# Optimization experiments

Hardware: AMD Instinct MI355X
Metric: run time of the kernel (lower is better)

## Reference

```python
import jax, jax.numpy as jnp
import numpy as np

EPS = 1e-5  # torch BatchNorm1d default eps
NUM_CLASSES = 10


def setup_inputs() -> dict:
    key = jax.random.key(0)
    ks = jax.random.split(key, 8)
    N, M, D = 8192, 8192, 256
    h1, h2 = 128, 64
    x = jax.random.normal(ks[0], (N, D), dtype=jnp.float32)
    x_n = jax.random.normal(ks[1], (M, D), dtype=jnp.float32)
    y_n = jax.random.randint(ks[2], (M,), 0, NUM_CLASSES)
    # Linear weights (torch layout [out, in]) and biases
    W0 = jax.random.normal(ks[3], (h1, D), dtype=jnp.float32) * 0.05
    b0 = jnp.zeros((h1,), dtype=jnp.float32)
    W1 = jax.random.normal(ks[4], (h2, h1), dtype=jnp.float32) * 0.05
    b1 = jnp.zeros((h2,), dtype=jnp.float32)
    # BatchNorm1d affine params (torch init: weight=1, bias=0)
    g0 = jnp.ones((h1,), dtype=jnp.float32)
    bt0 = jnp.zeros((h1,), dtype=jnp.float32)
    g1 = jnp.ones((h2,), dtype=jnp.float32)
    bt1 = jnp.zeros((h2,), dtype=jnp.float32)
    return {"x": x, "x_n": x_n, "y_n": y_n,
            "W0": W0, "b0": b0, "g0": g0, "bt0": bt0,
            "W1": W1, "b1": b1, "g1": g1, "bt1": bt1}


def _bn(h, gamma, beta):
    # BatchNorm1d in training mode: batch mean / biased batch var per feature
    m = jnp.mean(h, axis=0)
    v = jnp.var(h, axis=0)
    return gamma * (h - m) / jnp.sqrt(v + EPS) + beta


def _feats(z, params):
    # fcn stack: BatchNorm(Tanh(Linear(z)))
    for W, b, g, bt in params:
        z = _bn(jnp.tanh(z @ W.T + b), g, bt)
    return z


def reference(x, x_n, y_n, W0, b0, g0, bt0, W1, b1, g1, bt1):
    params = [(W0, b0, g0, bt0), (W1, b1, g1, bt1)]
    q = _feats(x, params)    # [N, 64]
    k = _feats(x_n, params)  # [M, 64]
    # euclidean cdist via the quadratic expansion
    d2 = (jnp.sum(q * q, axis=1)[:, None]
          + jnp.sum(k * k, axis=1)[None, :]
          - 2.0 * (q @ k.T))
    sim = jnp.sqrt(jnp.maximum(d2, 1e-12))  # [N, M]
    sim = jnp.max(sim) - sim                 # larger = nearer
    # x != x_n here, so no self-mask branch (matches torch.equal check)
    p = jax.nn.softmax(sim, axis=1)          # [N, M]
    y1h = jax.nn.one_hot(y_n, NUM_CLASSES, dtype=p.dtype)  # [M, C]
    return jnp.clip(p @ y1h, 0.0, 1.0)       # [N, C]
```

## Files before the change

### kernel.cpp

```cpp
#include <hip/hip_runtime.h>
#include <math.h>

#define EPSBN 1e-5f

typedef unsigned short u16;
typedef short bf16x8 __attribute__((ext_vector_type(8)));
typedef float f32x4 __attribute__((ext_vector_type(4)));
typedef int i32x4 __attribute__((ext_vector_type(4)));

constexpr int NROWS = 8192;
constexpr int D0 = 256;
constexpr int F1 = 128;
constexpr int F2 = 64;
constexpr int TOT = 2 * NROWS;
constexpr int NCLS = 10;
constexpr int MPAD = 8832;
constexpr int NT_PAD = MPAD / 64;
constexpr int GY = 12;

constexpr size_t OFF_W0P = 0;
constexpr size_t OFF_H1H = 32768;
constexpr size_t OFF_H1L = OFF_H1H + 1048576;
constexpr size_t OFF_P1S = OFF_H1L + 1048576;
constexpr size_t OFF_P1Q = OFF_P1S + 131072;
constexpr size_t OFF_SC0 = OFF_P1Q + 131072;
constexpr size_t OFF_SH0 = OFF_SC0 + 256;
constexpr size_t OFF_W1P = OFF_SH0 + 256;
constexpr size_t OFF_B1E = OFF_W1P + 16384;
constexpr size_t OFF_H2  = OFF_B1E + 128;
constexpr size_t OFF_P2S = OFF_H2 + 1048576;
constexpr size_t OFF_P2Q = OFF_P2S + 65536;
constexpr size_t OFF_SC1 = OFF_P2Q + 65536;
constexpr size_t OFF_SH1 = OFF_SC1 + 128;
constexpr size_t OFF_PIDX= OFF_SH1 + 128;
constexpr size_t OFF_TCLS= OFF_PIDX + MPAD;
constexpr size_t OFF_QH  = OFF_H1H;
constexpr size_t OFF_QL  = OFF_QH + 262144;
constexpr size_t OFF_QN2 = OFF_QL + 262144;
constexpr size_t OFF_KH  = OFF_QN2 + NROWS;
constexpr size_t OFF_KL  = OFF_KH + 282624;
constexpr size_t OFF_KN2 = OFF_KL + 282624;
constexpr size_t OFF_PART= OFF_H2;

__device__ inline u16 f2bf(float f) {
  unsigned u = __float_as_uint(f);
  unsigned r = (u + 0x7fffu + ((u >> 16) & 1u)) >> 16;
  return (u16)r;
}
__device__ inline float bf2f(u16 h) { return __uint_as_float(((unsigned)h) << 16); }

__device__ inline float tanh_fast(float x) {
  float e = __builtin_amdgcn_exp2f(x * 2.88539008f);
  return 1.f - 2.f * __builtin_amdgcn_rcpf(e + 1.f);
}

__global__ void k_w0pack(const float* __restrict__ w0, u16* __restrict__ w0p) {
  int idx = blockIdx.x * 256 + threadIdx.x;
  int j = idx >> 8, t = idx & 255;
  float v = w0[idx];
  u16 hi = f2bf(v);
  u16 lo = f2bf(v - bf2f(hi));
  w0p[(t >> 3) * 1024 + j * 8 + (t & 7)] = hi;
  w0p[32768 + (t >> 3) * 1024 + j * 8 + (t & 7)] = lo;
}

__global__ __launch_bounds__(256) void k_layer1(
    const float* __restrict__ x, const float* __restrict__ xn,
    const u16* __restrict__ w0p, const float* __restrict__ b0,
    u16* __restrict__ h1h, u16* __restrict__ h1l,
    float* __restrict__ p1s, float* __restrict__ p1q)
{
  const int tid = threadIdx.x;
  const int w = tid >> 6, l = tid & 63;
  const int l15 = l & 15, l4 = l >> 4;
  const int blk = blockIdx.x;
  const int rowHalf = w & 1, colHalf = w >> 1;
  const int r0 = blk * 32 + 16 * rowHalf;
  const int c0 = 64 * colHalf;
  const float* src = (blk < 256) ? (x + (size_t)blk * 32 * 256)
                                 : (xn + (size_t)(blk - 256) * 32 * 256);
  const float* xrow = src + (size_t)(16 * rowHalf + l15) * 256;

  f32x4 acc[4];
  #pragma unroll
  for (int ct = 0; ct < 4; ++ct) acc[ct] = (f32x4){0.f, 0.f, 0.f, 0.f};

  #pragma unroll
  for (int ks = 0; ks < 8; ++ks) {
    const float* xp = xrow + ks * 32 + l4 * 8;
    f32x4 a0 = *(const f32x4*)xp;
    f32x4 a1 = *(const f32x4*)(xp + 4);
    bf16x8 ah, al_;
    #pragma unroll
    for (int i = 0; i < 4; ++i) {
      u16 h = f2bf(a0[i]); ah[i] = (short)h; al_[i] = (short)f2bf(a0[i] - bf2f(h));
    }
    #pragma unroll
    for (int i = 0; i < 4; ++i) {
      u16 h = f2bf(a1[i]); ah[4 + i] = (short)h; al_[4 + i] = (short)f2bf(a1[i] - bf2f(h));
    }
    const u16* bbase = w0p + (size_t)(ks * 4 + l4) * 1024;
    #pragma unroll
    for (int ct = 0; ct < 4; ++ct) {
      const int col = c0 + 16 * ct + l15;
      bf16x8 bh = *(const bf16x8*)(bbase + col * 8);
      bf16x8 bl = *(const bf16x8*)(bbase + 32768 + col * 8);
      acc[ct] = __builtin_amdgcn_mfma_f32_16x16x32_bf16(ah, bh, acc[ct], 0, 0, 0);
      acc[ct] = __builtin_amdgcn_mfma_f32_16x16x32_bf16(ah, bl, acc[ct], 0, 0, 0);
      acc[ct] = __builtin_amdgcn_mfma_f32_16x16x32_bf16(al_, bh, acc[ct], 0, 0, 0);
    }
  }

  #pragma unroll
  for (int ct = 0; ct < 4; ++ct) {
    const int col = c0 + 16 * ct + l15;
    const float bj = b0[col];
    float s = 0.f, q = 0.f;
    #pragma unroll
    for (int r = 0; r < 4; ++r) {
      float v = tanh_fast(acc[ct][r] + bj);
      const int row = r0 + 4 * l4 + r;
      u16 hi = f2bf(v);
      h1h[(size_t)row * 128 + col] = hi;
      h1l[(size_t)row * 128 + col] = f2bf(v - bf2f(hi));
      s += v; q += v * v;
    }
    s += __shfl_xor(s, 16); s += __shfl_xor(s, 32);
    q += __shfl_xor(q, 16); q += __shfl_xor(q, 32);
    if (l < 16) {
      p1s[(size_t)(blk * 2 + rowHalf) * 128 + col] = s;
      p1q[(size_t)(blk * 2 + rowHalf) * 128 + col] = q;
    }
  }
}

__global__ __launch_bounds__(64) void k_red1(
    const float* __restrict__ p1s, const float* __restrict__ p1q,
    const float* __restrict__ g0, const float* __restrict__ bt0,
    float* __restrict__ sc0, float* __restrict__ sh0)
{
  const int b = blockIdx.x >> 7;
  const int j = blockIdx.x & 127;
  const int t = threadIdx.x;
  float s = 0.f, q = 0.f;
  for (int i = t; i < 512; i += 64) {
    s += p1s[(size_t)(b * 512 + i) * 128 + j];
    q += p1q[(size_t)(b * 512 + i) * 128 + j];
  }
  #pragma unroll
  for (int off = 32; off; off >>= 1) { s += __shfl_xor(s, off); q += __shfl_xor(q, off); }
  if (t == 0) {
    float m = s / (float)NROWS;
    float v = q / (float)NROWS - m * m;
    float sc = g0[j] * rsqrtf(v + EPSBN);
    sc0[b * 128 + j] = sc;
    sh0[b * 128 + j] = bt0[j] - m * sc;
  }
}

__global__ __launch_bounds__(128) void k_fold(
    const float* __restrict__ w1, const float* __restrict__ b1,
    const float* __restrict__ sc0, const float* __restrict__ sh0,
    u16* __restrict__ w1p, float* __restrict__ b1e)
{
  const int tid = threadIdx.x;
  const int b = tid >> 6, o = tid & 63;
  float acc = 0.f;
  for (int j = 0; j < 128; ++j) {
    float w = w1[o * 128 + j];
    float ws = w * sc0[b * 128 + j];
    acc += w * sh0[b * 128 + j];
    u16 hi = f2bf(ws);
    u16 lo = f2bf(ws - bf2f(hi));
    w1p[((size_t)(b * 2 + 0) * 16 + (j >> 3)) * 512 + o * 8 + (j & 7)] = hi;
    w1p[((size_t)(b * 2 + 1) * 16 + (j >> 3)) * 512 + o * 8 + (j & 7)] = lo;
  }
  b1e[b * 64 + o] = b1[o] + acc;
}

__global__ __launch_bounds__(256) void k_layer2(
    const u16* __restrict__ h1h, const u16* __restrict__ h1l,
    const u16* __restrict__ w1p, const float* __restrict__ b1e,
    float* __restrict__ h2, float* __restrict__ p2s, float* __restrict__ p2q)
{
  const int tid = threadIdx.x;
  const int w = tid >> 6, l = tid & 63;
  const int l15 = l & 15, l4 = l >> 4;
  const int blk = blockIdx.x;
  const int rowHalf = w & 1, colHalf = w >> 1;
  const int r0 = blk * 32 + 16 * rowHalf;
  const int c0 = 32 * colHalf;
  const int b = blk >> 8;
  const u16* arow_h = h1h + (size_t)(r0 + l15) * 128;
  const u16* arow_l = h1l + (size_t)(r0 + l15) * 128;

  f32x4 acc[2];
  acc[0] = (f32x4){0.f, 0.f, 0.f, 0.f};
  acc[1] = (f32x4){0.f, 0.f, 0.f, 0.f};

  #pragma unroll
  for (int ks = 0; ks < 4; ++ks) {
    bf16x8 ah = *(const bf16x8*)(arow_h + ks * 32 + l4 * 8);
    bf16x8 al_ = *(const bf16x8*)(arow_l + ks * 32 + l4 * 8);
    const u16* bb = w1p + ((size_t)(b * 2) * 16 + ks * 4 + l4) * 512;
    #pragma unroll
    for (int ct = 0; ct < 2; ++ct) {
      const int col = c0 + 16 * ct + l15;
      bf16x8 bh = *(const bf16x8*)(bb + col * 8);
      bf16x8 bl = *(const bf16x8*)(bb + 8192 + col * 8);
      acc[ct] = __builtin_amdgcn_mfma_f32_16x16x32_bf16(ah, bh, acc[ct], 0, 0, 0);
      acc[ct] = __builtin_amdgcn_mfma_f32_16x16x32_bf16(ah, bl, acc[ct], 0, 0, 0);
      acc[ct] = __builtin_amdgcn_mfma_f32_16x16x32_bf16(al_, bh, acc[ct], 0, 0, 0);
    }
  }

  #pragma unroll
  for (int ct = 0; ct < 2; ++ct) {
    const int col = c0 + 16 * ct + l15;
    const float bj = b1e[b * 64 + col];
    float s = 0.f, q = 0.f;
    #pragma unroll
    for (int r = 0; r < 4; ++r) {
      float v = tanh_fast(acc[ct][r] + bj);
      const int row = r0 + 4 * l4 + r;
      h2[(size_t)row * 64 + col] = v;
      s += v; q += v * v;
    }
    s += __shfl_xor(s, 16); s += __shfl_xor(s, 32);
    q += __shfl_xor(q, 16); q += __shfl_xor(q, 32);
    if (l < 16) {
      p2s[(size_t)(blk * 2 + rowHalf) * 64 + col] = s;
      p2q[(size_t)(blk * 2 + rowHalf) * 64 + col] = q;
    }
  }
}

__global__ __launch_bounds__(64) void k_red2(
    const float* __restrict__ p2s, const float* __restrict__ p2q,
    const float* __restrict__ g1, const float* __restrict__ bt1,
    float* __restrict__ sc1, float* __restrict__ sh1)
{
  const int b = blockIdx.x >> 6;
  const int o = blockIdx.x & 63;
  const int t = threadIdx.x;
  float s = 0.f, q = 0.f;
  for (int i = t; i < 512; i += 64) {
    s += p2s[(size_t)(b * 512 + i) * 64 + o];
    q += p2q[(size_t)(b * 512 + i) * 64 + o];
  }
  #pragma unroll
  for (int off = 32; off; off >>= 1) { s += __shfl_xor(s, off); q += __shfl_xor(q, off); }
  if (t == 0) {
    float m = s / (float)NROWS;
    float v = q / (float)NROWS - m * m;
    float sc = g1[o] * rsqrtf(v + EPSBN);
    sc1[b * 64 + o] = sc;
    sh1[b * 64 + o] = bt1[o] - m * sc;
  }
}

__global__ __launch_bounds__(256) void k_sort(const int* __restrict__ yn,
                                              int* __restrict__ pidx, int* __restrict__ tcls)
{
  __shared__ int cnt[256][NCLS];
  __shared__ int wtot[4][NCLS];
  __shared__ int pstart[NCLS + 1];
  const int t = threadIdx.x;
  const int lane = t & 63, w = t >> 6;
  #pragma unroll
  for (int c = 0; c < NCLS; ++c) cnt[t][c] = 0;
  for (int i = t; i < MPAD; i += 256) pidx[i] = -1;
  const int base = t * 32;
  for (int i = 0; i < 32; ++i) cnt[t][yn[base + i]]++;
  __syncthreads();
  #pragma unroll
  for (int c = 0; c < NCLS; ++c) {
    int x = cnt[t][c];
    int inc = x;
    #pragma unroll
    for (int d = 1; d < 64; d <<= 1) { int y = __shfl_up(inc, d); if (lane >= d) inc += y; }
    if (lane == 63) wtot[w][c] = inc;
    cnt[t][c] = inc - x;
  }
  __syncthreads();
  if (t == 0) {
    int run = 0;
    #pragma unroll
    for (int c = 0; c < NCLS; ++c) {
      int tot = wtot[0][c] + wtot[1][c] + wtot[2][c] + wtot[3][c];
      pstart[c] = run;
      int ntile = (tot + 63) >> 6;
      for (int tt = 0; tt < ntile; ++tt) tcls[(run >> 6) + tt] = c;
      run += ntile << 6;
    }
    pstart[NCLS] = run;
    for (int tt = run >> 6; tt < NT_PAD; ++tt) tcls[tt] = NCLS;
  }
  __syncthreads();
  #pragma unroll
  for (int c = 0; c < NCLS; ++c) {
    int add = pstart[c];
    for (int w2 = 0; w2 < 4; ++w2) if (w2 < w) add += wtot[w2][c];
    cnt[t][c] += add;
  }
  __syncthreads();
  for (int i = 0; i < 32; ++i) {
    int idx = base + i;
    int c = yn[idx];
    pidx[cnt[t][c]++] = idx;
  }
}

__global__ __launch_bounds__(256) void k_bn2(
    const float* __restrict__ h2, const float* __restrict__ sc1, const float* __restrict__ sh1,
    const int* __restrict__ pidx,
    u16* __restrict__ qh, u16* __restrict__ ql, float* __restrict__ qn2,
    u16* __restrict__ kh, u16* __restrict__ kl, float* __restrict__ kn2)
{
  const int tid = threadIdx.x;
  const int r = tid >> 6, o = tid & 63;
  if (blockIdx.x < 2048) {
    const int row = blockIdx.x * 4 + r;
    float v = sc1[o] * h2[(size_t)row * 64 + o] + sh1[o];
    u16 hi = f2bf(v);
    qh[(size_t)row * 64 + o] = hi;
    ql[(size_t)row * 64 + o] = f2bf(v - bf2f(hi));
    float sq = v * v;
    #pragma unroll
    for (int off = 32; off; off >>= 1) sq += __shfl_xor(sq, off);
    if (o == 0) qn2[row] = sq;
  } else {
    const int row = (blockIdx.x - 2048) * 4 + r;
    const int src = pidx[row];
    float v = 0.f;
    if (src >= 0) v = sc1[64 + o] * h2[(size_t)(NROWS + src) * 64 + o] + sh1[64 + o];
    u16 hi = f2bf(v);
    kh[(size_t)row * 64 + o] = hi;
    kl[(size_t)row * 64 + o] = f2bf(v - bf2f(hi));
    float sq = v * v;
    #pragma unroll
    for (int off = 32; off; off >>= 1) sq += __shfl_xor(sq, off);
    if (o == 0) kn2[row] = (src >= 0) ? sq : 1e30f;
  }
}

__global__ __launch_bounds__(256) void k_dist(
    const u16* __restrict__ qh, const u16* __restrict__ ql, const float* __restrict__ qn2,
    const u16* __restrict__ kh, const u16* __restrict__ kl, const float* __restrict__ kn2,
    const int* __restrict__ tcls, float* __restrict__ part)
{
  __shared__ u16 bs[64 * 128];
  __shared__ float cls_lds[(NCLS + 1) * 64];
  const int tid = threadIdx.x;
  const int l = tid & 63, w = tid >> 6;
  const int n0 = blockIdx.x * 64;
  const int g = blockIdx.y;
  const int t0 = g * 12;
  const int t1 = (t0 + 12 < NT_PAD) ? (t0 + 12) : NT_PAD;

  for (int i = tid; i < (NCLS + 1) * 64; i += 256) cls_lds[i] = 0.f;

  const int l15 = l & 15, l4 = l >> 4;
  const int arow = n0 + 16 * w + l15;
  const bf16x8 aH0 = *(const bf16x8*)(qh + (size_t)arow * 64 + l4 * 8);
  const bf16x8 aH1 = *(const bf16x8*)(qh + (size_t)arow * 64 + 32 + l4 * 8);
  const bf16x8 aL0 = *(const bf16x8*)(ql + (size_t)arow * 64 + l4 * 8);
  const bf16x8 aL1 = *(const bf16x8*)(ql + (size_t)arow * 64 + 32 + l4 * 8);
  const f32x4 qn = *(const f32x4*)(qn2 + n0 + 16 * w + l4 * 4);

  const ushort* arrp = ((tid >> 3) & 1) ? kl : kh;
  const int cp8 = (tid & 7) * 8;
  const int colb = tid >> 4;
  const int slot = ((tid >> 3) & 1) * 8 + ((tid & 7) ^ (colb & 7));
  char* dstb = (char*)bs + colb * 256 + slot * 16;

  const int P = l15 * 256 + ((l4 ^ (l & 7)) << 4);
  const char* bb = (const char*)bs;

  i32x4 st0, st1, st2, st3;
  {
    const int m0 = t0 * 64;
    st0 = *(const i32x4*)(arrp + (size_t)(m0 + colb) * 64 + cp8);
    st1 = *(const i32x4*)(arrp + (size_t)(m0 + 16 + colb) * 64 + cp8);
    st2 = *(const i32x4*)(arrp + (size_t)(m0 + 32 + colb) * 64 + cp8);
    st3 = *(const i32x4*)(arrp + (size_t)(m0 + 48 + colb) * 64 + cp8);
  }

  float run0 = 0.f, run1 = 0.f, run2 = 0.f, run3 = 0.f;
  int ccur = tcls[t0];

#define FLUSH(CC) { \
    run0 += __shfl_xor(run0, 1); run0 += __shfl_xor(run0, 2); run0 += __shfl_xor(run0, 4); run0 += __shfl_xor(run0, 8); \
    run1 += __shfl_xor(run1, 1); run1 += __shfl_xor(run1, 2); run1 += __shfl_xor(run1, 4); run1 += __shfl_xor(run1, 8); \
    run2 += __shfl_xor(run2, 1); run2 += __shfl_xor(run2, 2); run2 += __shfl_xor(run2, 4); run2 += __shfl_xor(run2, 8); \
    run3 += __shfl_xor(run3, 1); run3 += __shfl_xor(run3, 2); run3 += __shfl_xor(run3, 4); run3 += __shfl_xor(run3, 8); \
    if (l15 == 0) { \
      float* cl = cls_lds + (CC) * 64 + 16 * w + l4 * 4; \
      cl[0] += run0; cl[1] += run1; cl[2] += run2; cl[3] += run3; \
    } \
    run0 = run1 = run2 = run3 = 0.f; \
  }

#define CTSTEP(CT, ACC) { \
    const char* pp = bb + (CT) * 4096; \
    bf16x8 bh0 = *(const bf16x8*)(pp + P); \
    bf16x8 bh1 = *(const bf16x8*)(pp + (P ^ 64)); \
    bf16x8 bl0 = *(const bf16x8*)(pp + (P ^ 128)); \
    bf16x8 bl1 = *(const bf16x8*)(pp + (P ^ 192)); \
    ACC = __builtin_amdgcn_mfma_f32_16x16x32_bf16(aH0, bh0, ACC, 0, 0, 0); \
    ACC = __builtin_amdgcn_mfma_f32_16x16x32_bf16(aH1, bh1, ACC, 0, 0, 0); \
    ACC = __builtin_amdgcn_mfma_f32_16x16x32_bf16(aH0, bl0, ACC, 0, 0, 0); \
    ACC = __builtin_amdgcn_mfma_f32_16x16x32_bf16(aH1, bl1, ACC, 0, 0, 0); \
    ACC = __builtin_amdgcn_mfma_f32_16x16x32_bf16(aL0, bh0, ACC, 0, 0, 0); \
    ACC = __builtin_amdgcn_mfma_f32_16x16x32_bf16(aL1, bh1, ACC, 0, 0, 0); \
  }

#define EPI(ACC, KV) { \
    float d2, s_, u; \
    d2 = fmaxf(fmaf(-2.f, ACC[0], qn[0] + (KV)), 1e-12f); \
    s_ = __builtin_amdgcn_sqrtf(d2); \
    u = __builtin_amdgcn_exp2f(s_ * -1.44269504f); run0 += u; \
    d2 = fmaxf(fmaf(-2.f, ACC[1], qn[1] + (KV)), 1e-12f); \
    s_ = __builtin_amdgcn_sqrtf(d2); \
    u = __builtin_amdgcn_exp2f(s_ * -1.44269504f); run1 += u; \
    d2 = fmaxf(fmaf(-2.f, ACC[2], qn[2] + (KV)), 1e-12f); \
    s_ = __builtin_amdgcn_sqrtf(d2); \
    u = __builtin_amdgcn_exp2f(s_ * -1.44269504f); run2 += u; \
    d2 = fmaxf(fmaf(-2.f, ACC[3], qn[3] + (KV)), 1e-12f); \
    s_ = __builtin_amdgcn_sqrtf(d2); \
    u = __builtin_amdgcn_exp2f(s_ * -1.44269504f); run3 += u; \
  }

  for (int t = t0; t < t1; ++t) {
    const int m0 = t * 64;
    __syncthreads();
    *(i32x4*)(dstb)         = st0;
    *(i32x4*)(dstb + 4096)  = st1;
    *(i32x4*)(dstb + 8192)  = st2;
    *(i32x4*)(dstb + 12288) = st3;
    __syncthreads();
    if (t + 1 < t1) {
      const int m1 = m0 + 64;
      st0 = *(const i32x4*)(arrp + (size_t)(m1 + colb) * 64 + cp8);
      st1 = *(const i32x4*)(arrp + (size_t)(m1 + 16 + colb) * 64 + cp8);
      st2 = *(const i32x4*)(arrp + (size_t)(m1 + 32 + colb) * 64 + cp8);
      st3 = *(const i32x4*)(arrp + (size_t)(m1 + 48 + colb) * 64 + cp8);
    }
    const float kv0 = kn2[m0 + l15];
    const float kv1 = kn2[m0 + 16 + l15];
    const float kv2 = kn2[m0 + 32 + l15];
    const float kv3 = kn2[m0 + 48 + l15];
    const int c = tcls[t];
    if (c != ccur) { FLUSH(ccur); ccur = c; }

    f32x4 acc0 = {0.f, 0.f, 0.f, 0.f};
    f32x4 acc1 = {0.f, 0.f, 0.f, 0.f};
    f32x4 acc2 = {0.f, 0.f, 0.f, 0.f};
    f32x4 acc3 = {0.f, 0.f, 0.f, 0.f};
    CTSTEP(0, acc0)
    CTSTEP(1, acc1)
    CTSTEP(2, acc2)
    CTSTEP(3, acc3)
    EPI(acc0, kv0)
    EPI(acc1, kv1)
    EPI(acc2, kv2)
    EPI(acc3, kv3)
  }
  FLUSH(ccur);
  __syncthreads();

  for (int i = tid; i < (NCLS + 1) * 64; i += 256) {
    const int c = i >> 6, r = i & 63;
    part[((size_t)g * (NCLS + 1) + c) * NROWS + n0 + r] = cls_lds[i];
  }
#undef FLUSH
#undef CTSTEP
#undef EPI
}

__global__ __launch_bounds__(256) void k_final(const float* __restrict__ part,
                                               float* __restrict__ out)
{
  const int n = blockIdx.x * 256 + threadIdx.x;
  float sc[NCLS];
  #pragma unroll
  for (int c = 0; c < NCLS; ++c) sc[c] = 0.f;
  for (int g = 0; g < GY; ++g) {
    #pragma unroll
    for (int c = 0; c < NCLS; ++c)
      sc[c] += part[((size_t)g * (NCLS + 1) + c) * NROWS + n];
  }
  float tot = 0.f;
  #pragma unroll
  for (int c = 0; c < NCLS; ++c) tot += sc[c];
  const float inv = 1.f / tot;
  #pragma unroll
  for (int c = 0; c < NCLS; ++c)
    out[(size_t)n * NCLS + c] = fminf(fmaxf(sc[c] * inv, 0.f), 1.f);
}

extern "C" void kernel_launch(void* const* d_in, const int* in_sizes, int n_in,
                              void* d_out, int out_size, void* d_ws, size_t ws_size,
                              hipStream_t stream) {
  const float* x   = (const float*)d_in[0];
  const float* xn  = (const float*)d_in[1];
  const int*   yn  = (const int*)d_in[2];
  const float* W0  = (const float*)d_in[3];
  const float* b0  = (const float*)d_in[4];
  const float* g0  = (const float*)d_in[5];
  const float* bt0 = (const float*)d_in[6];
  const float* W1  = (const float*)d_in[7];
  const float* b1  = (const float*)d_in[8];
  const float* g1  = (const float*)d_in[9];
  const float* bt1 = (const float*)d_in[10];
  float* out = (float*)d_out;
  float* ws  = (float*)d_ws;

  u16*   w0pp = (u16*)(ws + OFF_W0P);
  u16*   h1hp = (u16*)(ws + OFF_H1H);
  u16*   h1lp = (u16*)(ws + OFF_H1L);
  float* p1sp = ws + OFF_P1S;
  float* p1qp = ws + OFF_P1Q;
  float* sc0p = ws + OFF_SC0;
  float* sh0p = ws + OFF_SH0;
  u16*   w1pp = (u16*)(ws + OFF_W1P);
  float* b1ep = ws + OFF_B1E;
  float* h2p  = ws + OFF_H2;
  float* p2sp = ws + OFF_P2S;
  float* p2qp = ws + OFF_P2Q;
  float* sc1p = ws + OFF_SC1;
  float* sh1p = ws + OFF_SH1;
  int*   pidxp= (int*)(ws + OFF_PIDX);
  int*   tclsp= (int*)(ws + OFF_TCLS);
  u16*   qhp  = (u16*)(ws + OFF_QH);
  u16*   qlp  = (u16*)(ws + OFF_QL);
  float* qn2p = ws + OFF_QN2;
  u16*   khp  = (u16*)(ws + OFF_KH);
  u16*   klp  = (u16*)(ws + OFF_KL);
  float* kn2p = ws + OFF_KN2;
  float* partp= ws + OFF_PART;

  k_sort<<<1, 256, 0, stream>>>(yn, pidxp, tclsp);
  k_w0pack<<<128, 256, 0, stream>>>(W0, w0pp);
  k_layer1<<<512, 256, 0, stream>>>(x, xn, w0pp, b0, h1hp, h1lp, p1sp, p1qp);
  k_red1<<<256, 64, 0, stream>>>(p1sp, p1qp, g0, bt0, sc0p, sh0p);
  k_fold<<<1, 128, 0, stream>>>(W1, b1, sc0p, sh0p, w1pp, b1ep);
  k_layer2<<<512, 256, 0, stream>>>(h1hp, h1lp, w1pp, b1ep, h2p, p2sp, p2qp);
  k_red2<<<128, 64, 0, stream>>>(p2sp, p2qp, g1, bt1, sc1p, sh1p);
  k_bn2<<<2048 + MPAD / 4, 256, 0, stream>>>(h2p, sc1p, sh1p, pidxp,
                                             qhp, qlp, qn2p, khp, klp, kn2p);
  k_dist<<<dim3(128, GY), 256, 0, stream>>>(qhp, qlp, qn2p, khp, klp, kn2p, tclsp, partp);
  k_final<<<32, 256, 0, stream>>>(partp, out);
}
```

Measured before the change: 152.6 us.

## Fuse prep kernels, atomic BN stats, and retile distance kernel to 32x32 MFMA

Merges the label sort and W0 packing into one prep kernel. BatchNorm partial sums are now accumulated with atomics, which removes both reduction kernels, and the fold is parallelised across 64 blocks. The distance kernel moves to 32x32x16 MFMA tiles with double-buffered LDS staging and a prefetch two tiles ahead, halves the grid's y-dimension, and folds the log2(e) scale into the norms so the epilogue needs one exp2 without a multiply. The costs are float atomics, which make the summation order nondeterministic, and more registers per thread, with occupancy capped at 3 blocks.

```diff
diff --git a/kernel.cpp b/kernel.cpp
--- a/kernel.cpp
+++ b/kernel.cpp
@@ -2,45 +2,39 @@
 #include <math.h>
 
 #define EPSBN 1e-5f
+#define AADD(p, v) __hip_atomic_fetch_add((p), (v), __ATOMIC_RELAXED, __HIP_MEMORY_SCOPE_AGENT)
 
 typedef unsigned short u16;
 typedef short bf16x8 __attribute__((ext_vector_type(8)));
 typedef float f32x4 __attribute__((ext_vector_type(4)));
+typedef float f32x16 __attribute__((ext_vector_type(16)));
 typedef int i32x4 __attribute__((ext_vector_type(4)));
 
 constexpr int NROWS = 8192;
-constexpr int D0 = 256;
-constexpr int F1 = 128;
-constexpr int F2 = 64;
-constexpr int TOT = 2 * NROWS;
 constexpr int NCLS = 10;
 constexpr int MPAD = 8832;
-constexpr int NT_PAD = MPAD / 64;
-constexpr int GY = 12;
+constexpr int NT_PAD = 138;
+constexpr int GY = 6;
+constexpr int TPG = 23;
+constexpr float SCL  = 2.0813689810056077f;
+constexpr float SCL2 = -4.1627379620112154f;
 
 constexpr size_t OFF_W0P = 0;
 constexpr size_t OFF_H1H = 32768;
 constexpr size_t OFF_H1L = OFF_H1H + 1048576;
-constexpr size_t OFF_P1S = OFF_H1L + 1048576;
-constexpr size_t OFF_P1Q = OFF_P1S + 131072;
-constexpr size_t OFF_SC0 = OFF_P1Q + 131072;
-constexpr size_t OFF_SH0 = OFF_SC0 + 256;
-constexpr size_t OFF_W1P = OFF_SH0 + 256;
+constexpr size_t OFF_SUM = OFF_H1L + 1048576;
+constexpr size_t OFF_W1P = OFF_SUM + 768;
 constexpr size_t OFF_B1E = OFF_W1P + 16384;
 constexpr size_t OFF_H2  = OFF_B1E + 128;
-constexpr size_t OFF_P2S = OFF_H2 + 1048576;
-constexpr size_t OFF_P2Q = OFF_P2S + 65536;
-constexpr size_t OFF_SC1 = OFF_P2Q + 65536;
-constexpr size_t OFF_SH1 = OFF_SC1 + 128;
-constexpr size_t OFF_PIDX= OFF_SH1 + 128;
-constexpr size_t OFF_TCLS= OFF_PIDX + MPAD;
+constexpr size_t OFF_PIDX = OFF_H2 + 1048576;
+constexpr size_t OFF_TCLS = OFF_PIDX + MPAD;
 constexpr size_t OFF_QH  = OFF_H1H;
 constexpr size_t OFF_QL  = OFF_QH + 262144;
 constexpr size_t OFF_QN2 = OFF_QL + 262144;
 constexpr size_t OFF_KH  = OFF_QN2 + NROWS;
 constexpr size_t OFF_KL  = OFF_KH + 282624;
 constexpr size_t OFF_KN2 = OFF_KL + 282624;
-constexpr size_t OFF_PART= OFF_H2;
+constexpr size_t OFF_PART = OFF_H2;
 
 __device__ inline u16 f2bf(float f) {
   unsigned u = __float_as_uint(f);
@@ -54,21 +48,74 @@
   return 1.f - 2.f * __builtin_amdgcn_rcpf(e + 1.f);
 }
 
-__global__ void k_w0pack(const float* __restrict__ w0, u16* __restrict__ w0p) {
-  int idx = blockIdx.x * 256 + threadIdx.x;
-  int j = idx >> 8, t = idx & 255;
-  float v = w0[idx];
-  u16 hi = f2bf(v);
-  u16 lo = f2bf(v - bf2f(hi));
-  w0p[(t >> 3) * 1024 + j * 8 + (t & 7)] = hi;
-  w0p[32768 + (t >> 3) * 1024 + j * 8 + (t & 7)] = lo;
+__global__ __launch_bounds__(256) void k_prep(
+    const float* __restrict__ w0, const int* __restrict__ yn,
+    u16* __restrict__ w0p, int* __restrict__ pidx, int* __restrict__ tcls,
+    float* __restrict__ sums)
+{
+  if (blockIdx.x < 128) {
+    int idx = blockIdx.x * 256 + threadIdx.x;
+    int t = idx & 255;
+    float v = w0[idx];
+    u16 hi = f2bf(v);
+    u16 lo = f2bf(v - bf2f(hi));
+    int j = idx >> 8;
+    w0p[(t >> 3) * 1024 + j * 8 + (t & 7)] = hi;
+    w0p[32768 + (t >> 3) * 1024 + j * 8 + (t & 7)] = lo;
+    return;
+  }
+  __shared__ int cnt[256][NCLS];
+  __shared__ int wtot[4][NCLS];
+  __shared__ int pstart[NCLS + 1];
+  const int t = threadIdx.x;
+  const int lane = t & 63, wv = t >> 6;
+  sums[t] = 0.f; sums[t + 256] = 0.f; sums[t + 512] = 0.f;
+  #pragma unroll
+  for (int c = 0; c < NCLS; ++c) cnt[t][c] = 0;
+  for (int i = t; i < MPAD; i += 256) pidx[i] = -1;
+  for (int i = t; i < NROWS; i += 256) cnt[t][yn[i]]++;
+  __syncthreads();
+  #pragma unroll
+  for (int c = 0; c < NCLS; ++c) {
+    int x = cnt[t][c];
+    int inc = x;
+    #pragma unroll
+    for (int d = 1; d < 64; d <<= 1) { int y = __shfl_up(inc, d); if (lane >= d) inc += y; }
+    if (lane == 63) wtot[wv][c] = inc;
+    cnt[t][c] = inc - x;
+  }
+  __syncthreads();
+  if (t == 0) {
+    int run = 0;
+    #pragma unroll
+    for (int c = 0; c < NCLS; ++c) {
+      int tot = wtot[0][c] + wtot[1][c] + wtot[2][c] + wtot[3][c];
+      pstart[c] = run;
+      int ntile = (tot + 63) >> 6;
+      for (int tt = 0; tt < ntile; ++tt) tcls[(run >> 6) + tt] = c;
+      run += ntile << 6;
+    }
+    pstart[NCLS] = run;
+    for (int tt = run >> 6; tt < NT_PAD; ++tt) tcls[tt] = NCLS;
+  }
+  __syncthreads();
+  #pragma unroll
+  for (int c = 0; c < NCLS; ++c) {
+    int add = pstart[c];
+    for (int w2 = 0; w2 < 4; ++w2) if (w2 < wv) add += wtot[w2][c];
+    cnt[t][c] += add;
+  }
+  __syncthreads();
+  for (int i = t; i < NROWS; i += 256) {
+    int c = yn[i];
+    pidx[cnt[t][c]++] = i;
+  }
 }
 
 __global__ __launch_bounds__(256) void k_layer1(
     const float* __restrict__ x, const float* __restrict__ xn,
     const u16* __restrict__ w0p, const float* __restrict__ b0,
-    u16* __restrict__ h1h, u16* __restrict__ h1l,
-    float* __restrict__ p1s, float* __restrict__ p1q)
+    u16* __restrict__ h1h, u16* __restrict__ h1l, float* __restrict__ sums)
 {
   const int tid = threadIdx.x;
   const int w = tid >> 6, l = tid & 63;
@@ -77,6 +124,7 @@
   const int rowHalf = w & 1, colHalf = w >> 1;
   const int r0 = blk * 32 + 16 * rowHalf;
   const int c0 = 64 * colHalf;
+  const int b = (blk < 256) ? 0 : 1;
   const float* src = (blk < 256) ? (x + (size_t)blk * 32 * 256)
                                  : (xn + (size_t)(blk - 256) * 32 * 256);
   const float* xrow = src + (size_t)(16 * rowHalf + l15) * 256;
@@ -128,60 +176,46 @@
     s += __shfl_xor(s, 16); s += __shfl_xor(s, 32);
     q += __shfl_xor(q, 16); q += __shfl_xor(q, 32);
     if (l < 16) {
-      p1s[(size_t)(blk * 2 + rowHalf) * 128 + col] = s;
-      p1q[(size_t)(blk * 2 + rowHalf) * 128 + col] = q;
-    }
-  }
-}
-
-__global__ __launch_bounds__(64) void k_red1(
-    const float* __restrict__ p1s, const float* __restrict__ p1q,
+      AADD(&sums[b * 128 + col], s);
+      AADD(&sums[256 + b * 128 + col], q);
+    }
+  }
+}
+
+__global__ __launch_bounds__(128) void k_foldp(
+    const float* __restrict__ w1, const float* __restrict__ b1,
     const float* __restrict__ g0, const float* __restrict__ bt0,
-    float* __restrict__ sc0, float* __restrict__ sh0)
-{
-  const int b = blockIdx.x >> 7;
-  const int j = blockIdx.x & 127;
-  const int t = threadIdx.x;
-  float s = 0.f, q = 0.f;
-  for (int i = t; i < 512; i += 64) {
-    s += p1s[(size_t)(b * 512 + i) * 128 + j];
-    q += p1q[(size_t)(b * 512 + i) * 128 + j];
-  }
-  #pragma unroll
-  for (int off = 32; off; off >>= 1) { s += __shfl_xor(s, off); q += __shfl_xor(q, off); }
-  if (t == 0) {
-    float m = s / (float)NROWS;
-    float v = q / (float)NROWS - m * m;
+    const float* __restrict__ sums, u16* __restrict__ w1p, float* __restrict__ b1e)
+{
+  const int o = blockIdx.x;
+  const int j = threadIdx.x;
+  __shared__ float red[2][2];
+  const float w = w1[o * 128 + j];
+  #pragma unroll
+  for (int b = 0; b < 2; ++b) {
+    float s = sums[b * 128 + j], q = sums[256 + b * 128 + j];
+    float m = s * (1.f / 8192.f);
+    float v = q * (1.f / 8192.f) - m * m;
     float sc = g0[j] * rsqrtf(v + EPSBN);
-    sc0[b * 128 + j] = sc;
-    sh0[b * 128 + j] = bt0[j] - m * sc;
-  }
-}
-
-__global__ __launch_bounds__(128) void k_fold(
-    const float* __restrict__ w1, const float* __restrict__ b1,
-    const float* __restrict__ sc0, const float* __restrict__ sh0,
-    u16* __restrict__ w1p, float* __restrict__ b1e)
-{
-  const int tid = threadIdx.x;
-  const int b = tid >> 6, o = tid & 63;
-  float acc = 0.f;
-  for (int j = 0; j < 128; ++j) {
-    float w = w1[o * 128 + j];
-    float ws = w * sc0[b * 128 + j];
-    acc += w * sh0[b * 128 + j];
-    u16 hi = f2bf(ws);
-    u16 lo = f2bf(ws - bf2f(hi));
+    float sh = bt0[j] - m * sc;
+    float wsc = w * sc;
+    u16 hi = f2bf(wsc);
+    u16 lo = f2bf(wsc - bf2f(hi));
     w1p[((size_t)(b * 2 + 0) * 16 + (j >> 3)) * 512 + o * 8 + (j & 7)] = hi;
     w1p[((size_t)(b * 2 + 1) * 16 + (j >> 3)) * 512 + o * 8 + (j & 7)] = lo;
-  }
-  b1e[b * 64 + o] = b1[o] + acc;
+    float a = w * sh;
+    #pragma unroll
+    for (int off = 32; off; off >>= 1) a += __shfl_xor(a, off);
+    if ((j & 63) == 0) red[j >> 6][b] = a;
+  }
+  __syncthreads();
+  if (j < 2) b1e[j * 64 + o] = b1[o] + red[0][j] + red[1][j];
 }
 
 __global__ __launch_bounds__(256) void k_layer2(
     const u16* __restrict__ h1h, const u16* __restrict__ h1l,
     const u16* __restrict__ w1p, const float* __restrict__ b1e,
-    float* __restrict__ h2, float* __restrict__ p2s, float* __restrict__ p2q)
+    float* __restrict__ h2, float* __restrict__ sums)
 {
   const int tid = threadIdx.x;
   const int w = tid >> 6, l = tid & 63;
@@ -229,253 +263,163 @@
     s += __shfl_xor(s, 16); s += __shfl_xor(s, 32);
     q += __shfl_xor(q, 16); q += __shfl_xor(q, 32);
     if (l < 16) {
-      p2s[(size_t)(blk * 2 + rowHalf) * 64 + col] = s;
-      p2q[(size_t)(blk * 2 + rowHalf) * 64 + col] = q;
-    }
-  }
-}
-
-__global__ __launch_bounds__(64) void k_red2(
-    const float* __restrict__ p2s, const float* __restrict__ p2q,
+      AADD(&sums[512 + b * 64 + col], s);
+      AADD(&sums[640 + b * 64 + col], q);
+    }
+  }
+}
+
+__global__ __launch_bounds__(256) void k_bn2(
+    const float* __restrict__ h2, const float* __restrict__ sums,
     const float* __restrict__ g1, const float* __restrict__ bt1,
-    float* __restrict__ sc1, float* __restrict__ sh1)
-{
-  const int b = blockIdx.x >> 6;
-  const int o = blockIdx.x & 63;
-  const int t = threadIdx.x;
-  float s = 0.f, q = 0.f;
-  for (int i = t; i < 512; i += 64) {
-    s += p2s[(size_t)(b * 512 + i) * 64 + o];
-    q += p2q[(size_t)(b * 512 + i) * 64 + o];
-  }
-  #pragma unroll
-  for (int off = 32; off; off >>= 1) { s += __shfl_xor(s, off); q += __shfl_xor(q, off); }
-  if (t == 0) {
-    float m = s / (float)NROWS;
-    float v = q / (float)NROWS - m * m;
-    float sc = g1[o] * rsqrtf(v + EPSBN);
-    sc1[b * 64 + o] = sc;
-    sh1[b * 64 + o] = bt1[o] - m * sc;
-  }
-}
-
-__global__ __launch_bounds__(256) void k_sort(const int* __restrict__ yn,
-                                              int* __restrict__ pidx, int* __restrict__ tcls)
-{
-  __shared__ int cnt[256][NCLS];
-  __shared__ int wtot[4][NCLS];
-  __shared__ int pstart[NCLS + 1];
-  const int t = threadIdx.x;
-  const int lane = t & 63, w = t >> 6;
-  #pragma unroll
-  for (int c = 0; c < NCLS; ++c) cnt[t][c] = 0;
-  for (int i = t; i < MPAD; i += 256) pidx[i] = -1;
-  const int base = t * 32;
-  for (int i = 0; i < 32; ++i) cnt[t][yn[base + i]]++;
-  __syncthreads();
-  #pragma unroll
-  for (int c = 0; c < NCLS; ++c) {
-    int x = cnt[t][c];
-    int inc = x;
-    #pragma unroll
-    for (int d = 1; d < 64; d <<= 1) { int y = __shfl_up(inc, d); if (lane >= d) inc += y; }
-    if (lane == 63) wtot[w][c] = inc;
-    cnt[t][c] = inc - x;
-  }
-  __syncthreads();
-  if (t == 0) {
-    int run = 0;
-    #pragma unroll
-    for (int c = 0; c < NCLS; ++c) {
-      int tot = wtot[0][c] + wtot[1][c] + wtot[2][c] + wtot[3][c];
-      pstart[c] = run;
-      int ntile = (tot + 63) >> 6;
-      for (int tt = 0; tt < ntile; ++tt) tcls[(run >> 6) + tt] = c;
-      run += ntile << 6;
-    }
-    pstart[NCLS] = run;
-    for (int tt = run >> 6; tt < NT_PAD; ++tt) tcls[tt] = NCLS;
-  }
-  __syncthreads();
-  #pragma unroll
-  for (int c = 0; c < NCLS; ++c) {
-    int add = pstart[c];
-    for (int w2 = 0; w2 < 4; ++w2) if (w2 < w) add += wtot[w2][c];
-    cnt[t][c] += add;
-  }
-  __syncthreads();
-  for (int i = 0; i < 32; ++i) {
-    int idx = base + i;
-    int c = yn[idx];
-    pidx[cnt[t][c]++] = idx;
-  }
-}
-
-__global__ __launch_bounds__(256) void k_bn2(
-    const float* __restrict__ h2, const float* __restrict__ sc1, const float* __restrict__ sh1,
     const int* __restrict__ pidx,
     u16* __restrict__ qh, u16* __restrict__ ql, float* __restrict__ qn2,
     u16* __restrict__ kh, u16* __restrict__ kl, float* __restrict__ kn2)
 {
   const int tid = threadIdx.x;
   const int r = tid >> 6, o = tid & 63;
-  if (blockIdx.x < 2048) {
+  const bool isq = (blockIdx.x < 2048);
+  const int b = isq ? 0 : 1;
+  float s = sums[512 + b * 64 + o], q = sums[640 + b * 64 + o];
+  float m = s * (1.f / 8192.f);
+  float v = q * (1.f / 8192.f) - m * m;
+  float sc = g1[o] * rsqrtf(v + EPSBN);
+  float sh = bt1[o] - m * sc;
+  if (isq) {
     const int row = blockIdx.x * 4 + r;
-    float v = sc1[o] * h2[(size_t)row * 64 + o] + sh1[o];
-    u16 hi = f2bf(v);
+    float vv = sc * h2[(size_t)row * 64 + o] + sh;
+    u16 hi = f2bf(vv);
     qh[(size_t)row * 64 + o] = hi;
-    ql[(size_t)row * 64 + o] = f2bf(v - bf2f(hi));
-    float sq = v * v;
+    ql[(size_t)row * 64 + o] = f2bf(vv - bf2f(hi));
+    float sq = vv * vv;
     #pragma unroll
     for (int off = 32; off; off >>= 1) sq += __shfl_xor(sq, off);
-    if (o == 0) qn2[row] = sq;
+    if (o == 0) qn2[row] = SCL * sq;
   } else {
     const int row = (blockIdx.x - 2048) * 4 + r;
     const int src = pidx[row];
-    float v = 0.f;
-    if (src >= 0) v = sc1[64 + o] * h2[(size_t)(NROWS + src) * 64 + o] + sh1[64 + o];
-    u16 hi = f2bf(v);
+    float vv = 0.f;
+    if (src >= 0) vv = sc * h2[(size_t)(NROWS + src) * 64 + o] + sh;
+    u16 hi = f2bf(vv);
     kh[(size_t)row * 64 + o] = hi;
-    kl[(size_t)row * 64 + o] = f2bf(v - bf2f(hi));
-    float sq = v * v;
+    kl[(size_t)row * 64 + o] = f2bf(vv - bf2f(hi));
+    float sq = vv * vv;
     #pragma unroll
     for (int off = 32; off; off >>= 1) sq += __shfl_xor(sq, off);
-    if (o == 0) kn2[row] = (src >= 0) ? sq : 1e30f;
-  }
-}
-
-__global__ __launch_bounds__(256) void k_dist(
+    if (o == 0) kn2[row] = (src >= 0) ? SCL * sq : 1e30f;
+  }
+}
+
+__global__ __launch_bounds__(256, 3) void k_dist(
     const u16* __restrict__ qh, const u16* __restrict__ ql, const float* __restrict__ qn2,
     const u16* __restrict__ kh, const u16* __restrict__ kl, const float* __restrict__ kn2,
     const int* __restrict__ tcls, float* __restrict__ part)
 {
-  __shared__ u16 bs[64 * 128];
-  __shared__ float cls_lds[(NCLS + 1) * 64];
+  __shared__ u16 bs[2][8192];
+  __shared__ float cls_lds[2 * (NCLS + 1) * 64];
   const int tid = threadIdx.x;
-  const int l = tid & 63, w = tid >> 6;
+  const int w = tid >> 6, l = tid & 63;
   const int n0 = blockIdx.x * 64;
   const int g = blockIdx.y;
-  const int t0 = g * 12;
-  const int t1 = (t0 + 12 < NT_PAD) ? (t0 + 12) : NT_PAD;
-
-  for (int i = tid; i < (NCLS + 1) * 64; i += 256) cls_lds[i] = 0.f;
-
-  const int l15 = l & 15, l4 = l >> 4;
-  const int arow = n0 + 16 * w + l15;
-  const bf16x8 aH0 = *(const bf16x8*)(qh + (size_t)arow * 64 + l4 * 8);
-  const bf16x8 aH1 = *(const bf16x8*)(qh + (size_t)arow * 64 + 32 + l4 * 8);
-  const bf16x8 aL0 = *(const bf16x8*)(ql + (size_t)arow * 64 + l4 * 8);
-  const bf16x8 aL1 = *(const bf16x8*)(ql + (size_t)arow * 64 + 32 + l4 * 8);
-  const f32x4 qn = *(const f32x4*)(qn2 + n0 + 16 * w + l4 * 4);
-
-  const ushort* arrp = ((tid >> 3) & 1) ? kl : kh;
-  const int cp8 = (tid & 7) * 8;
-  const int colb = tid >> 4;
-  const int slot = ((tid >> 3) & 1) * 8 + ((tid & 7) ^ (colb & 7));
-  char* dstb = (char*)bs + colb * 256 + slot * 16;
-
-  const int P = l15 * 256 + ((l4 ^ (l & 7)) << 4);
-  const char* bb = (const char*)bs;
+  const int t0 = g * TPG, t1 = t0 + TPG;
+
+  for (int i = tid; i < 2 * (NCLS + 1) * 64; i += 256) cls_lds[i] = 0.f;
+
+  const int lh = l >> 5;
+  const int arow = n0 + 32 * (w >> 1) + (l & 31);
+  bf16x8 aH[4], aL[4];
+  #pragma unroll
+  for (int j = 0; j < 4; ++j) {
+    aH[j] = *(const bf16x8*)(qh + (size_t)arow * 64 + j * 16 + 8 * lh);
+    aL[j] = *(const bf16x8*)(ql + (size_t)arow * 64 + j * 16 + 8 * lh);
+  }
+  float qnr[16];
+  #pragma unroll
+  for (int g4 = 0; g4 < 4; ++g4) {
+    f32x4 qv = *(const f32x4*)(qn2 + n0 + 32 * (w >> 1) + 8 * g4 + 4 * lh);
+    qnr[4 * g4 + 0] = qv[0]; qnr[4 * g4 + 1] = qv[1];
+    qnr[4 * g4 + 2] = qv[2]; qnr[4 * g4 + 3] = qv[3];
+  }
+
+  const int sarr = w & 1, shalf = w >> 1;
+  const u16* sbase = (sarr ? kl : kh) + (size_t)l * 64 + shalf * 32;
+  const int c7l = l & 7;
+  char* wb_base = (char*)&bs[0][0] + l * 256 + sarr * 128;
+  const int ws0 = (((shalf * 4 + 0) ^ c7l) << 4);
+  const int ws1 = (((shalf * 4 + 1) ^ c7l) << 4);
+  const int ws2 = (((shalf * 4 + 2) ^ c7l) << 4);
+  const int ws3 = (((shalf * 4 + 3) ^ c7l) << 4);
+
+  const int colL = 32 * (w & 1) + (l & 31);
+  const char* rb_base = (const char*)&bs[0][0] + colL * 256;
+  const int c7r = colL & 7;
 
   i32x4 st0, st1, st2, st3;
-  {
-    const int m0 = t0 * 64;
-    st0 = *(const i32x4*)(arrp + (size_t)(m0 + colb) * 64 + cp8);
-    st1 = *(const i32x4*)(arrp + (size_t)(m0 + 16 + colb) * 64 + cp8);
-    st2 = *(const i32x4*)(arrp + (size_t)(m0 + 32 + colb) * 64 + cp8);
-    st3 = *(const i32x4*)(arrp + (size_t)(m0 + 48 + colb) * 64 + cp8);
-  }
-
-  float run0 = 0.f, run1 = 0.f, run2 = 0.f, run3 = 0.f;
+#define LOADST(TT) do { const u16* sp_ = sbase + (size_t)(TT) * 4096; \
+    st0 = *(const i32x4*)(sp_);      st1 = *(const i32x4*)(sp_ + 8);  \
+    st2 = *(const i32x4*)(sp_ + 16); st3 = *(const i32x4*)(sp_ + 24); } while (0)
+#define WRITEST(PB) do { char* d_ = wb_base + (PB) * 16384; \
+    *(i32x4*)(d_ + ws0) = st0; *(i32x4*)(d_ + ws1) = st1; \
+    *(i32x4*)(d_ + ws2) = st2; *(i32x4*)(d_ + ws3) = st3; } while (0)
+#define FLUSH(CC) do { \
+    _Pragma("unroll") for (int r = 0; r < 16; ++r) { \
+      run[r] += __shfl_xor(run[r], 1);  run[r] += __shfl_xor(run[r], 2); \
+      run[r] += __shfl_xor(run[r], 4);  run[r] += __shfl_xor(run[r], 8); \
+      run[r] += __shfl_xor(run[r], 16); } \
+    if ((l & 31) == 0) { \
+      float* cl_ = cls_lds + (w & 1) * 704 + (CC) * 64 + 32 * (w >> 1) + 4 * lh; \
+      _Pragma("unroll") for (int r = 0; r < 16; ++r) cl_[(r & 3) + 8 * (r >> 2)] += run[r]; } \
+    _Pragma("unroll") for (int r = 0; r < 16; ++r) run[r] = 0.f; } while (0)
+
+  LOADST(t0);
+  WRITEST(0);
+  LOADST(t0 + 1);
+
+  float run[16];
+  #pragma unroll
+  for (int r = 0; r < 16; ++r) run[r] = 0.f;
   int ccur = tcls[t0];
-
-#define FLUSH(CC) { \
-    run0 += __shfl_xor(run0, 1); run0 += __shfl_xor(run0, 2); run0 += __shfl_xor(run0, 4); run0 += __shfl_xor(run0, 8); \
-    run1 += __shfl_xor(run1, 1); run1 += __shfl_xor(run1, 2); run1 += __shfl_xor(run1, 4); run1 += __shfl_xor(run1, 8); \
-    run2 += __shfl_xor(run2, 1); run2 += __shfl_xor(run2, 2); run2 += __shfl_xor(run2, 4); run2 += __shfl_xor(run2, 8); \
-    run3 += __shfl_xor(run3, 1); run3 += __shfl_xor(run3, 2); run3 += __shfl_xor(run3, 4); run3 += __shfl_xor(run3, 8); \
-    if (l15 == 0) { \
-      float* cl = cls_lds + (CC) * 64 + 16 * w + l4 * 4; \
-      cl[0] += run0; cl[1] += run1; cl[2] += run2; cl[3] += run3; \
-    } \
-    run0 = run1 = run2 = run3 = 0.f; \
-  }
-
-#define CTSTEP(CT, ACC) { \
-    const char* pp = bb + (CT) * 4096; \
-    bf16x8 bh0 = *(const bf16x8*)(pp + P); \
-    bf16x8 bh1 = *(const bf16x8*)(pp + (P ^ 64)); \
-    bf16x8 bl0 = *(const bf16x8*)(pp + (P ^ 128)); \
-    bf16x8 bl1 = *(const bf16x8*)(pp + (P ^ 192)); \
-    ACC = __builtin_amdgcn_mfma_f32_16x16x32_bf16(aH0, bh0, ACC, 0, 0, 0); \
-    ACC = __builtin_amdgcn_mfma_f32_16x16x32_bf16(aH1, bh1, ACC, 0, 0, 0); \
-    ACC = __builtin_amdgcn_mfma_f32_16x16x32_bf16(aH0, bl0, ACC, 0, 0, 0); \
-    ACC = __builtin_amdgcn_mfma_f32_16x16x32_bf16(aH1, bl1, ACC, 0, 0, 0); \
-    ACC = __builtin_amdgcn_mfma_f32_16x16x32_bf16(aL0, bh0, ACC, 0, 0, 0); \
-    ACC = __builtin_amdgcn_mfma_f32_16x16x32_bf16(aL1, bh1, ACC, 0, 0, 0); \
-  }
-
-#define EPI(ACC, KV) { \
-    float d2, s_, u; \
-    d2 = fmaxf(fmaf(-2.f, ACC[0], qn[0] + (KV)), 1e-12f); \
-    s_ = __builtin_amdgcn_sqrtf(d2); \
-    u = __builtin_amdgcn_exp2f(s_ * -1.44269504f); run0 += u; \
-    d2 = fmaxf(fmaf(-2.f, ACC[1], qn[1] + (KV)), 1e-12f); \
-    s_ = __builtin_amdgcn_sqrtf(d2); \
-    u = __builtin_amdgcn_exp2f(s_ * -1.44269504f); run1 += u; \
-    d2 = fmaxf(fmaf(-2.f, ACC[2], qn[2] + (KV)), 1e-12f); \
-    s_ = __builtin_amdgcn_sqrtf(d2); \
-    u = __builtin_amdgcn_exp2f(s_ * -1.44269504f); run2 += u; \
-    d2 = fmaxf(fmaf(-2.f, ACC[3], qn[3] + (KV)), 1e-12f); \
-    s_ = __builtin_amdgcn_sqrtf(d2); \
-    u = __builtin_amdgcn_exp2f(s_ * -1.44269504f); run3 += u; \
-  }
+  int p = 0;
 
   for (int t = t0; t < t1; ++t) {
-    const int m0 = t * 64;
     __syncthreads();
-    *(i32x4*)(dstb)         = st0;
-    *(i32x4*)(dstb + 4096)  = st1;
-    *(i32x4*)(dstb + 8192)  = st2;
-    *(i32x4*)(dstb + 12288) = st3;
-    __syncthreads();
-    if (t + 1 < t1) {
-      const int m1 = m0 + 64;
-      st0 = *(const i32x4*)(arrp + (size_t)(m1 + colb) * 64 + cp8);
-      st1 = *(const i32x4*)(arrp + (size_t)(m1 + 16 + colb) * 64 + cp8);
-      st2 = *(const i32x4*)(arrp + (size_t)(m1 + 32 + colb) * 64 + cp8);
-      st3 = *(const i32x4*)(arrp + (size_t)(m1 + 48 + colb) * 64 + cp8);
-    }
-    const float kv0 = kn2[m0 + l15];
-    const float kv1 = kn2[m0 + 16 + l15];
-    const float kv2 = kn2[m0 + 32 + l15];
-    const float kv3 = kn2[m0 + 48 + l15];
+    if (t + 1 < t1) WRITEST(p ^ 1);
+    if (t + 2 < t1) LOADST(t + 2);
     const int c = tcls[t];
     if (c != ccur) { FLUSH(ccur); ccur = c; }
-
-    f32x4 acc0 = {0.f, 0.f, 0.f, 0.f};
-    f32x4 acc1 = {0.f, 0.f, 0.f, 0.f};
-    f32x4 acc2 = {0.f, 0.f, 0.f, 0.f};
-    f32x4 acc3 = {0.f, 0.f, 0.f, 0.f};
-    CTSTEP(0, acc0)
-    CTSTEP(1, acc1)
-    CTSTEP(2, acc2)
-    CTSTEP(3, acc3)
-    EPI(acc0, kv0)
-    EPI(acc1, kv1)
-    EPI(acc2, kv2)
-    EPI(acc3, kv3)
+    const float kv = kn2[t * 64 + colL];
+
+    f32x16 acc;
+    #pragma unroll
+    for (int r = 0; r < 16; ++r) acc[r] = 0.f;
+    const char* pb = rb_base + p * 16384;
+    #pragma unroll
+    for (int j = 0; j < 4; ++j) {
+      const int c8 = 2 * j + lh;
+      bf16x8 bh  = *(const bf16x8*)(pb + ((c8 ^ c7r) << 4));
+      bf16x8 bl_ = *(const bf16x8*)(pb + 128 + ((c8 ^ c7r) << 4));
+      acc = __builtin_amdgcn_mfma_f32_32x32x16_bf16(aH[j], bh,  acc, 0, 0, 0);
+      acc = __builtin_amdgcn_mfma_f32_32x32x16_bf16(aH[j], bl_, acc, 0, 0, 0);
+      acc = __builtin_amdgcn_mfma_f32_32x32x16_bf16(aL[j], bh,  acc, 0, 0, 0);
+    }
+    #pragma unroll
+    for (int r = 0; r < 16; ++r) {
+      float d2 = fmaf(SCL2, acc[r], qnr[r] + kv);
+      d2 = fmaxf(d2, 2.0813689e-12f);
+      run[r] += __builtin_amdgcn_exp2f(-__builtin_amdgcn_sqrtf(d2));
+    }
+    p ^= 1;
   }
   FLUSH(ccur);
   __syncthreads();
 
   for (int i = tid; i < (NCLS + 1) * 64; i += 256) {
-    const int c = i >> 6, r = i & 63;
-    part[((size_t)g * (NCLS + 1) + c) * NROWS + n0 + r] = cls_lds[i];
-  }
+    const int c = i >> 6, rr = i & 63;
+    part[((size_t)g * (NCLS + 1) + c) * NROWS + n0 + rr] = cls_lds[i] + cls_lds[704 + i];
+  }
+#undef LOADST
+#undef WRITEST
 #undef FLUSH
-#undef CTSTEP
-#undef EPI
 }
 
 __global__ __launch_bounds__(256) void k_final(const float* __restrict__ part,
@@ -519,17 +463,10 @@
   u16*   w0pp = (u16*)(ws + OFF_W0P);
   u16*   h1hp = (u16*)(ws + OFF_H1H);
   u16*   h1lp = (u16*)(ws + OFF_H1L);
-  float* p1sp = ws + OFF_P1S;
-  float* p1qp = ws + OFF_P1Q;
-  float* sc0p = ws + OFF_SC0;
-  float* sh0p = ws + OFF_SH0;
+  float* sumsp= ws + OFF_SUM;
   u16*   w1pp = (u16*)(ws + OFF_W1P);
   float* b1ep = ws + OFF_B1E;
   float* h2p  = ws + OFF_H2;
-  float* p2sp = ws + OFF_P2S;
-  float* p2qp = ws + OFF_P2Q;
-  float* sc1p = ws + OFF_SC1;
-  float* sh1p = ws + OFF_SH1;
   int*   pidxp= (int*)(ws + OFF_PIDX);
   int*   tclsp= (int*)(ws + OFF_TCLS);
   u16*   qhp  = (u16*)(ws + OFF_QH);
@@ -540,14 +477,11 @@
   float* kn2p = ws + OFF_KN2;
   float* partp= ws + OFF_PART;
 
-  k_sort<<<1, 256, 0, stream>>>(yn, pidxp, tclsp);
-  k_w0pack<<<128, 256, 0, stream>>>(W0, w0pp);
-  k_layer1<<<512, 256, 0, stream>>>(x, xn, w0pp, b0, h1hp, h1lp, p1sp, p1qp);
-  k_red1<<<256, 64, 0, stream>>>(p1sp, p1qp, g0, bt0, sc0p, sh0p);
-  k_fold<<<1, 128, 0, stream>>>(W1, b1, sc0p, sh0p, w1pp, b1ep);
-  k_layer2<<<512, 256, 0, stream>>>(h1hp, h1lp, w1pp, b1ep, h2p, p2sp, p2qp);
-  k_red2<<<128, 64, 0, stream>>>(p2sp, p2qp, g1, bt1, sc1p, sh1p);
-  k_bn2<<<2048 + MPAD / 4, 256, 0, stream>>>(h2p, sc1p, sh1p, pidxp,
+  k_prep<<<129, 256, 0, stream>>>(W0, yn, w0pp, pidxp, tclsp, sumsp);
+  k_layer1<<<512, 256, 0, stream>>>(x, xn, w0pp, b0, h1hp, h1lp, sumsp);
+  k_foldp<<<64, 128, 0, stream>>>(W1, b1, g0, bt0, sumsp, w1pp, b1ep);
+  k_layer2<<<512, 256, 0, stream>>>(h1hp, h1lp, w1pp, b1ep, h2p, sumsp);
+  k_bn2<<<2048 + MPAD / 4, 256, 0, stream>>>(h2p, sumsp, g1, bt1, pidxp,
                                              qhp, qlp, qn2p, khp, klp, kn2p);
   k_dist<<<dim3(128, GY), 256, 0, stream>>>(qhp, qlp, qn2p, khp, klp, kn2p, tclsp, partp);
   k_final<<<32, 256, 0, stream>>>(partp, out);
```

New measurement: 137.4 us. 1.11x faster.
